# Kernel tuning notes

Hardware: AMD Instinct MI355X
Metric: run time of the kernel (lower is better)

Reference implementation:

```python
import jax, jax.numpy as jnp
import numpy as np

B, S, D, H = 2, 2048, 1024, 16
DH = D // H  # 64


def setup_inputs() -> dict:
    key = jax.random.key(0)
    ks = jax.random.split(key, 6)
    scale = 1.0 / np.sqrt(D)
    x = jax.random.normal(ks[0], (B, S, D), dtype=jnp.float32)
    Wq = jax.random.normal(ks[1], (D, D), dtype=jnp.float32) * scale
    Wk = jax.random.normal(ks[2], (D, D), dtype=jnp.float32) * scale
    Wv = jax.random.normal(ks[3], (D, D), dtype=jnp.float32) * scale
    Wo = jax.random.normal(ks[4], (D, D), dtype=jnp.float32) * scale
    zeros = jnp.zeros((D,), dtype=jnp.float32)
    return {"x": x, "Wq": Wq, "bq": zeros, "Wk": Wk, "bk": zeros,
            "Wv": Wv, "bv": zeros, "Wo": Wo, "bo": zeros}


def reference(x, Wq, bq, Wk, bk, Wv, bv, Wo, bo):
    # x: [B, S, D]
    def split_heads(t):
        # [B, S, D] -> [B, H, S, DH]
        return t.reshape(B, S, H, DH).transpose(0, 2, 1, 3)

    q = split_heads(x @ Wq + bq)
    k = split_heads(x @ Wk + bk)
    v = split_heads(x @ Wv + bv)

    scores = jnp.einsum('bhqd,bhkd->bhqk', q, k) / jnp.sqrt(jnp.float32(DH))
    weights = jax.nn.softmax(scores, axis=-1)          # [B, H, S, S]
    o = jnp.einsum('bhqk,bhkd->bhqd', weights, v)       # [B, H, S, DH]
    o = o.transpose(0, 2, 1, 3).reshape(B, S, D)        # merge heads
    return o @ Wo + bo
```

## Files before the change

### kernel.cpp

```cpp
#include <hip/hip_runtime.h>
#include <hip/hip_bf16.h>

#define DEV __device__ __forceinline__

typedef short bf16x8 __attribute__((ext_vector_type(8)));
typedef float f32x4 __attribute__((ext_vector_type(4)));
typedef unsigned int u32;
typedef unsigned int u32x4 __attribute__((ext_vector_type(4)));

constexpr int BB = 2, SS = 2048, DD = 1024, HH = 16, DHD = 64;
constexpr int MM = BB * SS;
#define QSC 0.1803368801111f

#if __has_builtin(__builtin_amdgcn_exp2f)
#define EXP2(x) __builtin_amdgcn_exp2f(x)
#else
#define EXP2(x) exp2f(x)
#endif

DEV unsigned short f2bf(float f) {
    union { float f; unsigned int u; } v; v.f = f;
    return (unsigned short)((v.u + 0x8000u) >> 16);
}
#if __has_builtin(__builtin_amdgcn_perm)
DEV u32 pk2bf(float a, float b) {
    union { float f; u32 u; } ua, ub; ua.f = a; ub.f = b;
    return __builtin_amdgcn_perm(ub.u + 0x8000u, ua.u + 0x8000u, 0x07060302u);
}
#else
DEV u32 pk2bf(float a, float b) {
    union { float f; u32 u; } ua, ub; ua.f = a; ub.f = b;
    return ((ua.u + 0x8000u) >> 16) | ((ub.u + 0x8000u) & 0xffff0000u);
}
#endif

DEV u32 cvtpk2bf(float a, float b) {
    u32 r;
    asm("v_cvt_pk_bf16_f32 %0, %1, %2" : "=v"(r) : "v"(a), "v"(b));
    return r;
}

DEV bf16x8 ld_bf16x8(const unsigned short* p) { return *(const bf16x8*)p; }

DEV void gl16(const unsigned short* g, unsigned short* l) {
    __builtin_amdgcn_global_load_lds(
        (const __attribute__((address_space(1))) u32*)g,
        (__attribute__((address_space(3))) u32*)l, 16, 0, 0);
}

__global__ void prep(const float* __restrict__ x, unsigned short* __restrict__ xb,
                     const float* __restrict__ W0, const float* __restrict__ W1,
                     const float* __restrict__ W2, const float* __restrict__ W3,
                     unsigned short* __restrict__ WtBase) {
    __shared__ float tile[32][33];
    int blk = blockIdx.x;
    if (blk < 4096) {
        int i = blk * 256 + threadIdx.x;
        float4 v = ((const float4*)x)[i];
        uint2 o;
        o.x = pk2bf(v.x, v.y);
        o.y = pk2bf(v.z, v.w);
        ((uint2*)xb)[i] = o;
        return;
    }
    blk -= 4096;
    int wsel = blk >> 10;
    const float* W = (wsel == 0) ? W0 : (wsel == 1) ? W1 : (wsel == 2) ? W2 : W3;
    unsigned short* Wt = WtBase + (size_t)wsel * DD * DD;
    int t = blk & 1023;
    int n0 = (t & 31) * 32, k0 = (t >> 5) * 32;
    int tx = threadIdx.x & 31, ty = threadIdx.x >> 5;
    #pragma unroll
    for (int i = 0; i < 4; ++i)
        tile[ty + 8 * i][tx] = W[(size_t)(k0 + ty + 8 * i) * DD + n0 + tx];
    __syncthreads();
    #pragma unroll
    for (int i = 0; i < 4; ++i)
        Wt[(size_t)(n0 + ty + 8 * i) * DD + k0 + tx] = f2bf(tile[tx][ty + 8 * i]);
}

__global__ __launch_bounds__(512, 2) void qkv_gemm(
    const unsigned short* __restrict__ xb,
    const unsigned short* __restrict__ WtBase,
    const float* __restrict__ bq, const float* __restrict__ bk, const float* __restrict__ bv,
    unsigned short* __restrict__ Qb, unsigned short* __restrict__ Kb, unsigned short* __restrict__ Vt)
{
    __shared__ __align__(16) unsigned short AL[3][128 * 32];
    __shared__ __align__(16) unsigned short BL[3][3][128 * 32];

    const int gid2 = blockIdx.x + 8 * blockIdx.y;
    const int xk = gid2 & 7, o = gid2 >> 3;
    const int xe = (xk & 1) * 4 + (o & 3);
    const int ye = (xk >> 1) * 8 + (o >> 2);
    const int m0g = ye * 128;
    const int n0g = xe * 128;

    const int wave = threadIdx.x >> 6, lane = threadIdx.x & 63;
    const int quad = lane >> 4, lcol = lane & 15;
    const int wr = wave >> 2, wc = wave & 3;

    f32x4 acc[3][4][2];
    #pragma unroll
    for (int z = 0; z < 3; ++z)
        #pragma unroll
        for (int i = 0; i < 4; ++i)
            #pragma unroll
            for (int j = 0; j < 2; ++j) acc[z][i][j] = (f32x4){0.f, 0.f, 0.f, 0.f};

    auto stage = [&](int ks, int bf) {
        int bi = threadIdx.x;
        int row = bi >> 2, p = (bi & 3) ^ ((row >> 1) & 3);
        gl16(xb + (size_t)(m0g + row) * DD + ks + p * 8, &AL[bf][wave * 512]);
        #pragma unroll
        for (int z = 0; z < 3; ++z)
            gl16(WtBase + (size_t)z * DD * DD + (size_t)(n0g + row) * DD + ks + p * 8,
                 &BL[bf][z][wave * 512]);
    };

    auto compute = [&](int bf) {
        bf16x8 af[4];
        #pragma unroll
        for (int mt = 0; mt < 4; ++mt) {
            int row = wr * 64 + mt * 16 + lcol;
            af[mt] = ld_bf16x8(&AL[bf][(row * 4 + (quad ^ ((row >> 1) & 3))) * 8]);
        }
        #pragma unroll
        for (int z = 0; z < 3; ++z) {
            bf16x8 bz[2];
            #pragma unroll
            for (int nt = 0; nt < 2; ++nt) {
                int row = wc * 32 + nt * 16 + lcol;
                bz[nt] = ld_bf16x8(&BL[bf][z][(row * 4 + (quad ^ ((row >> 1) & 3))) * 8]);
            }
            if (z < 2) {
                #pragma unroll
                for (int mt = 0; mt < 4; ++mt)
                    #pragma unroll
                    for (int nt = 0; nt < 2; ++nt)
                        acc[z][mt][nt] = __builtin_amdgcn_mfma_f32_16x16x32_bf16(bz[nt], af[mt], acc[z][mt][nt], 0, 0, 0);
            } else {
                #pragma unroll
                for (int mt = 0; mt < 4; ++mt)
                    #pragma unroll
                    for (int nt = 0; nt < 2; ++nt)
                        acc[z][mt][nt] = __builtin_amdgcn_mfma_f32_16x16x32_bf16(af[mt], bz[nt], acc[z][mt][nt], 0, 0, 0);
            }
        }
    };

    stage(0, 0);
    stage(32, 1);

    for (int kk = 0; kk < 30; kk += 3) {
        #pragma unroll
        for (int u = 0; u < 3; ++u) {
            int k = kk + u;
            stage((k + 2) * 32, (u + 2) % 3);
            asm volatile("s_waitcnt vmcnt(8)" ::: "memory");
            __builtin_amdgcn_s_barrier();
            __builtin_amdgcn_sched_barrier(0);
            compute(u);
            __builtin_amdgcn_s_barrier();
        }
    }
    asm volatile("s_waitcnt vmcnt(4)" ::: "memory");
    __builtin_amdgcn_s_barrier();
    __builtin_amdgcn_sched_barrier(0);
    compute(0);
    __builtin_amdgcn_s_barrier();
    asm volatile("s_waitcnt vmcnt(0)" ::: "memory");
    __builtin_amdgcn_s_barrier();
    __builtin_amdgcn_sched_barrier(0);
    compute(1);

    #pragma unroll
    for (int z = 0; z < 2; ++z) {
        unsigned short* dst = (z == 0) ? Qb : Kb;
        const float sc = (z == 0) ? QSC : 1.0f;
        const float* bias = (z == 0) ? bq : bk;
        #pragma unroll
        for (int mt = 0; mt < 4; ++mt) {
            int m = m0g + wr * 64 + mt * 16 + lcol;
            int b_ = m >> 11, s = m & (SS - 1);
            #pragma unroll
            for (int nt = 0; nt < 2; ++nt) {
                int nbt = n0g + wc * 32 + nt * 16 + quad * 4;
                int h = nbt >> 6, dh0 = nbt & 63;
                float4 bv4 = *(const float4*)&bias[nbt];
                uint2 o2;
                o2.x = pk2bf((acc[z][mt][nt][0] + bv4.x) * sc, (acc[z][mt][nt][1] + bv4.y) * sc);
                o2.y = pk2bf((acc[z][mt][nt][2] + bv4.z) * sc, (acc[z][mt][nt][3] + bv4.w) * sc);
                *(uint2*)&dst[(((size_t)b_ * HH + h) * SS + s) * DHD + dh0] = o2;
            }
        }
    }
    #pragma unroll
    for (int mt = 0; mt < 4; ++mt) {
        int mbt = m0g + wr * 64 + mt * 16 + quad * 4;
        int b_ = mbt >> 11, s0 = mbt & (SS - 1);
        #pragma unroll
        for (int nt = 0; nt < 2; ++nt) {
            int n = n0g + wc * 32 + nt * 16 + lcol;
            int h = n >> 6, dh = n & 63;
            float bvv = bv[n];
            uint2 o2;
            o2.x = pk2bf(acc[2][mt][nt][0] + bvv, acc[2][mt][nt][1] + bvv);
            o2.y = pk2bf(acc[2][mt][nt][2] + bvv, acc[2][mt][nt][3] + bvv);
            *(uint2*)&Vt[(((size_t)b_ * HH + h) * DHD + dh) * SS + s0] = o2;
        }
    }
}

__global__ __launch_bounds__(512, 4) void attn(
    const unsigned short* __restrict__ Qb,
    const unsigned short* __restrict__ Kb,
    const unsigned short* __restrict__ Vt,
    unsigned short* __restrict__ Ob)
{
    __shared__ __align__(16) unsigned short Kld[2][64 * 64];
    __shared__ __align__(16) unsigned short Vld[2][64 * 64];

    const int g = blockIdx.y * gridDim.x + blockIdx.x;
    const int bh = (g & 7) * 4 + ((g >> 3) & 3);
    const int qt = g >> 5;
    const int b = bh >> 4, h = bh & (HH - 1);
    const unsigned short* Qbh = Qb + (size_t)bh * SS * DHD;
    const unsigned short* Kbh = Kb + (size_t)bh * SS * DHD;
    const unsigned short* Vbh = Vt + (size_t)bh * DHD * SS;

    const int wave = threadIdx.x >> 6, lane = threadIdx.x & 63;
    const int quad = lane >> 4, lcol = lane & 15;
    const int rowbase = qt * 128 + wave * 16;

    bf16x8 qf0 = ld_bf16x8(Qbh + (size_t)(rowbase + lcol) * DHD + quad * 8);
    bf16x8 qf1 = ld_bf16x8(Qbh + (size_t)(rowbase + lcol) * DHD + 32 + quad * 8);

    auto krow = [&](int kf2, int j) {
        return kf2 * 32 + ((lcol >> 2) << 3) + j * 4 + (lcol & 3);
    };
    auto kswz = [](int r) { return (r & 3) | (((r >> 3) & 1) << 2); };

    auto stage = [&](int c, int bf) {
        int kb = c * 64;
        #pragma unroll
        for (int i = 0; i < 2; ++i) {
            int j = wave * 2 + i;
            if (j < 8) {
                int bi = j * 64 + lane;
                int r = bi >> 3, p = (bi & 7) ^ ((r & 3) | (((r >> 3) & 1) << 2));
                gl16(Kbh + (size_t)(kb + r) * DHD + p * 8, &Kld[bf][j * 512]);
            } else {
                int jj = j - 8;
                int bi = jj * 64 + lane;
                int dh = bi >> 3, p = (bi & 7) ^ (dh & 7);
                gl16(Vbh + (size_t)dh * SS + kb + p * 8, &Vld[bf][jj * 512]);
            }
        }
    };

    stage(0, 0);
    __syncthreads();

    float m0 = -1e30f;
    #pragma unroll
    for (int kf2 = 0; kf2 < 2; ++kf2)
        #pragma unroll
        for (int j = 0; j < 2; ++j) {
            int kr = krow(kf2, j), sw = kswz(kr);
            bf16x8 ka0 = ld_bf16x8(&Kld[0][(kr * 8 + (quad ^ sw)) * 8]);
            bf16x8 ka1 = ld_bf16x8(&Kld[0][(kr * 8 + ((quad + 4) ^ sw)) * 8]);
            f32x4 s = (f32x4){0.f, 0.f, 0.f, 0.f};
            s = __builtin_amdgcn_mfma_f32_16x16x32_bf16(ka0, qf0, s, 0, 0, 0);
            s = __builtin_amdgcn_mfma_f32_16x16x32_bf16(ka1, qf1, s, 0, 0, 0);
            #pragma unroll
            for (int r = 0; r < 4; ++r) m0 = fmaxf(m0, s[r]);
        }
    #pragma unroll
    for (int msk = 1; msk < 64; msk <<= 1) m0 = fmaxf(m0, __shfl_xor(m0, msk, 64));
    const f32x4 minit = (f32x4){-m0, -m0, -m0, -m0};

    f32x4 oacc[4];
    #pragma unroll
    for (int nt = 0; nt < 4; ++nt) oacc[nt] = (f32x4){0.f, 0.f, 0.f, 0.f};
    float ps = 0.f;

    for (int c = 0; c < 32; ++c) {
        int bf = c & 1;
        if (c + 1 < 32) stage(c + 1, (c + 1) & 1);

        bf16x8 paf[2];
        #pragma unroll
        for (int kf2 = 0; kf2 < 2; ++kf2) {
            u32 w[4];
            #pragma unroll
            for (int j = 0; j < 2; ++j) {
                int kr = krow(kf2, j), sw = kswz(kr);
                bf16x8 ka0 = ld_bf16x8(&Kld[bf][(kr * 8 + (quad ^ sw)) * 8]);
                bf16x8 ka1 = ld_bf16x8(&Kld[bf][(kr * 8 + ((quad + 4) ^ sw)) * 8]);
                f32x4 s = minit;
                s = __builtin_amdgcn_mfma_f32_16x16x32_bf16(ka0, qf0, s, 0, 0, 0);
                s = __builtin_amdgcn_mfma_f32_16x16x32_bf16(ka1, qf1, s, 0, 0, 0);
                float e0 = EXP2(s[0]), e1 = EXP2(s[1]);
                float e2 = EXP2(s[2]), e3 = EXP2(s[3]);
                ps += (e0 + e1) + (e2 + e3);
                w[j * 2]     = cvtpk2bf(e0, e1);
                w[j * 2 + 1] = cvtpk2bf(e2, e3);
            }
            union { u32x4 u; bf16x8 v; } pu;
            pu.u = (u32x4){w[0], w[1], w[2], w[3]};
            paf[kf2] = pu.v;
        }

        #pragma unroll
        for (int kf2 = 0; kf2 < 2; ++kf2) {
            #pragma unroll
            for (int nt = 0; nt < 4; ++nt) {
                int dh = nt * 16 + lcol;
                bf16x8 vb = ld_bf16x8(&Vld[bf][(dh * 8 + ((kf2 * 4 + quad) ^ (dh & 7))) * 8]);
                oacc[nt] = __builtin_amdgcn_mfma_f32_16x16x32_bf16(paf[kf2], vb, oacc[nt], 0, 0, 0);
            }
        }
        __syncthreads();
    }

    ps += __shfl_xor(ps, 16, 64);
    ps += __shfl_xor(ps, 32, 64);
    float inv = 1.0f / ps;
    #pragma unroll
    for (int r = 0; r < 4; ++r) {
        float iv = __shfl(inv, quad * 4 + r, 64);
        int srow = rowbase + quad * 4 + r;
        size_t base = (((size_t)b * SS + srow) * HH + h) * DHD;
        #pragma unroll
        for (int nt = 0; nt < 4; ++nt)
            Ob[base + nt * 16 + lcol] = f2bf(oacc[nt][r] * iv);
    }
}

__global__ __launch_bounds__(256) void out_gemm(
    const unsigned short* __restrict__ Ob,
    const unsigned short* __restrict__ Wto,
    const float* __restrict__ bo,
    float* __restrict__ out)
{
    __shared__ __align__(16) unsigned short Wld[2][128 * 64];
    __shared__ __align__(16) unsigned short Old[2][64 * 64];

    const int m0g = blockIdx.y * 64;
    const int n0g = blockIdx.x * 128;
    const int wave = threadIdx.x >> 6, lane = threadIdx.x & 63;
    const int quad = lane >> 4, lcol = lane & 15;
    const int nb = wave * 32;

    f32x4 acc[2][4];
    #pragma unroll
    for (int i = 0; i < 2; ++i)
        #pragma unroll
        for (int j = 0; j < 4; ++j) acc[i][j] = (f32x4){0.f, 0.f, 0.f, 0.f};

    auto stage = [&](int ks, int bf) {
        #pragma unroll
        for (int i = 0; i < 6; ++i) {
            int j = wave * 6 + i;
            if (j < 16) {
                int bi = j * 64 + lane;
                int r = bi >> 3, p = (bi & 7) ^ (r & 7);
                gl16(Wto + (size_t)(n0g + r) * DD + ks + p * 8, &Wld[bf][j * 512]);
            } else {
                int jj = j - 16;
                int bi = jj * 64 + lane;
                int r = bi >> 3, p = (bi & 7) ^ (r & 7);
                gl16(Ob + (size_t)(m0g + r) * DD + ks + p * 8, &Old[bf][jj * 512]);
            }
        }
    };

    stage(0, 0);
    __syncthreads();

    for (int kk = 0; kk < 16; ++kk) {
        int bf = kk & 1;
        if (kk + 1 < 16) stage((kk + 1) * 64, (kk + 1) & 1);
        #pragma unroll
        for (int kh = 0; kh < 2; ++kh) {
            bf16x8 wf[2], of[4];
            #pragma unroll
            for (int i = 0; i < 2; ++i) {
                int row = nb + i * 16 + lcol;
                wf[i] = ld_bf16x8(&Wld[bf][(row * 8 + ((kh * 4 + quad) ^ (row & 7))) * 8]);
            }
            #pragma unroll
            for (int j = 0; j < 4; ++j) {
                int row = j * 16 + lcol;
                of[j] = ld_bf16x8(&Old[bf][(row * 8 + ((kh * 4 + quad) ^ (row & 7))) * 8]);
            }
            #pragma unroll
            for (int i = 0; i < 2; ++i)
                #pragma unroll
                for (int j = 0; j < 4; ++j)
                    acc[i][j] = __builtin_amdgcn_mfma_f32_16x16x32_bf16(wf[i], of[j], acc[i][j], 0, 0, 0);
        }
        __syncthreads();
    }

    #pragma unroll
    for (int i = 0; i < 2; ++i) {
        int n4 = n0g + nb + i * 16 + quad * 4;
        float4 bv4 = *(const float4*)&bo[n4];
        #pragma unroll
        for (int j = 0; j < 4; ++j) {
            int token = m0g + j * 16 + lcol;
            float4 o;
            o.x = acc[i][j][0] + bv4.x;
            o.y = acc[i][j][1] + bv4.y;
            o.z = acc[i][j][2] + bv4.z;
            o.w = acc[i][j][3] + bv4.w;
            *(float4*)&out[(size_t)token * DD + n4] = o;
        }
    }
}

extern "C" void kernel_launch(void* const* d_in, const int* in_sizes, int n_in,
                              void* d_out, int out_size, void* d_ws, size_t ws_size,
                              hipStream_t stream)
{
    const float* x  = (const float*)d_in[0];
    const float* Wq = (const float*)d_in[1];
    const float* bq = (const float*)d_in[2];
    const float* Wk = (const float*)d_in[3];
    const float* bk = (const float*)d_in[4];
    const float* Wv = (const float*)d_in[5];
    const float* bv = (const float*)d_in[6];
    const float* Wo = (const float*)d_in[7];
    const float* bo = (const float*)d_in[8];
    float* out = (float*)d_out;

    unsigned short* ws = (unsigned short*)d_ws;
    unsigned short* Wt  = ws;
    unsigned short* Wto = Wt + 3 * (size_t)DD * DD;
    unsigned short* Qb  = Wt + 4 * (size_t)DD * DD;
    unsigned short* Kb  = Qb + (size_t)MM * DD;
    unsigned short* Vt  = Kb + (size_t)MM * DD;
    unsigned short* xb  = Vt + (size_t)MM * DD;
    unsigned short* Ob  = xb;

    prep<<<8192, 256, 0, stream>>>(x, xb, Wq, Wk, Wv, Wo, Wt);

    qkv_gemm<<<dim3(8, 32), 512, 0, stream>>>(xb, Wt, bq, bk, bv, Qb, Kb, Vt);

    attn<<<dim3(16, 32), 512, 0, stream>>>(Qb, Kb, Vt, Ob);

    out_gemm<<<dim3(DD / 128, MM / 64), 256, 0, stream>>>(Ob, Wto, bo, out);
}
```

Before: 183.7 us.

## Split attention key chunk across wave pairs, each wave handling 32 query rows

After: 198.1 us. 7.8% more time.

```diff
diff --git a/kernel.cpp b/kernel.cpp
--- a/kernel.cpp
+++ b/kernel.cpp
@@ -219,6 +219,9 @@
 {
     __shared__ __align__(16) unsigned short Kld[2][64 * 64];
     __shared__ __align__(16) unsigned short Vld[2][64 * 64];
+    __shared__ float exch[8 * 16 * 64];
+    __shared__ float psx[8][2][16];
+    __shared__ float smax[8];
 
     const int g = blockIdx.y * gridDim.x + blockIdx.x;
     const int bh = (g & 7) * 4 + ((g >> 3) & 3);
@@ -230,13 +233,18 @@
 
     const int wave = threadIdx.x >> 6, lane = threadIdx.x & 63;
     const int quad = lane >> 4, lcol = lane & 15;
-    const int rowbase = qt * 128 + wave * 16;
-
-    bf16x8 qf0 = ld_bf16x8(Qbh + (size_t)(rowbase + lcol) * DHD + quad * 8);
-    bf16x8 qf1 = ld_bf16x8(Qbh + (size_t)(rowbase + lcol) * DHD + 32 + quad * 8);
-
-    auto krow = [&](int kf2, int j) {
-        return kf2 * 32 + ((lcol >> 2) << 3) + j * 4 + (lcol & 3);
+    const int qg = wave >> 1, kh = wave & 1;
+    const int rowbase = qt * 128 + qg * 32;
+
+    bf16x8 qf0[2], qf1[2];
+    #pragma unroll
+    for (int g2 = 0; g2 < 2; ++g2) {
+        qf0[g2] = ld_bf16x8(Qbh + (size_t)(rowbase + g2 * 16 + lcol) * DHD + quad * 8);
+        qf1[g2] = ld_bf16x8(Qbh + (size_t)(rowbase + g2 * 16 + lcol) * DHD + 32 + quad * 8);
+    }
+
+    auto krow = [&](int j) {
+        return kh * 32 + ((lcol >> 2) << 3) + j * 4 + (lcol & 3);
     };
     auto kswz = [](int r) { return (r & 3) | (((r >> 3) & 1) << 2); };
 
@@ -260,80 +268,109 @@
 
     stage(0, 0);
     __syncthreads();
-
-    float m0 = -1e30f;
-    #pragma unroll
-    for (int kf2 = 0; kf2 < 2; ++kf2)
+    {
+        float m0 = -1e30f;
         #pragma unroll
         for (int j = 0; j < 2; ++j) {
-            int kr = krow(kf2, j), sw = kswz(kr);
+            int kr = krow(j), sw = kswz(kr);
             bf16x8 ka0 = ld_bf16x8(&Kld[0][(kr * 8 + (quad ^ sw)) * 8]);
             bf16x8 ka1 = ld_bf16x8(&Kld[0][(kr * 8 + ((quad + 4) ^ sw)) * 8]);
-            f32x4 s = (f32x4){0.f, 0.f, 0.f, 0.f};
-            s = __builtin_amdgcn_mfma_f32_16x16x32_bf16(ka0, qf0, s, 0, 0, 0);
-            s = __builtin_amdgcn_mfma_f32_16x16x32_bf16(ka1, qf1, s, 0, 0, 0);
-            #pragma unroll
-            for (int r = 0; r < 4; ++r) m0 = fmaxf(m0, s[r]);
-        }
-    #pragma unroll
-    for (int msk = 1; msk < 64; msk <<= 1) m0 = fmaxf(m0, __shfl_xor(m0, msk, 64));
-    const f32x4 minit = (f32x4){-m0, -m0, -m0, -m0};
-
-    f32x4 oacc[4];
-    #pragma unroll
-    for (int nt = 0; nt < 4; ++nt) oacc[nt] = (f32x4){0.f, 0.f, 0.f, 0.f};
-    float ps = 0.f;
+            #pragma unroll
+            for (int g2 = 0; g2 < 2; ++g2) {
+                f32x4 s = (f32x4){0.f, 0.f, 0.f, 0.f};
+                s = __builtin_amdgcn_mfma_f32_16x16x32_bf16(ka0, qf0[g2], s, 0, 0, 0);
+                s = __builtin_amdgcn_mfma_f32_16x16x32_bf16(ka1, qf1[g2], s, 0, 0, 0);
+                #pragma unroll
+                for (int r = 0; r < 4; ++r) m0 = fmaxf(m0, s[r]);
+            }
+        }
+        #pragma unroll
+        for (int msk = 1; msk < 64; msk <<= 1) m0 = fmaxf(m0, __shfl_xor(m0, msk, 64));
+        if (lane == 0) smax[wave] = m0;
+    }
+    __syncthreads();
+    float m0b = smax[0];
+    #pragma unroll
+    for (int w2 = 1; w2 < 8; ++w2) m0b = fmaxf(m0b, smax[w2]);
+    const f32x4 minit = (f32x4){-m0b, -m0b, -m0b, -m0b};
+
+    f32x4 oacc[2][4];
+    #pragma unroll
+    for (int g2 = 0; g2 < 2; ++g2)
+        #pragma unroll
+        for (int nt = 0; nt < 4; ++nt) oacc[g2][nt] = (f32x4){0.f, 0.f, 0.f, 0.f};
+    float ps0 = 0.f, ps1 = 0.f;
 
     for (int c = 0; c < 32; ++c) {
         int bf = c & 1;
         if (c + 1 < 32) stage(c + 1, (c + 1) & 1);
 
+        bf16x8 ka0[2], ka1[2];
+        #pragma unroll
+        for (int j = 0; j < 2; ++j) {
+            int kr = krow(j), sw = kswz(kr);
+            ka0[j] = ld_bf16x8(&Kld[bf][(kr * 8 + (quad ^ sw)) * 8]);
+            ka1[j] = ld_bf16x8(&Kld[bf][(kr * 8 + ((quad + 4) ^ sw)) * 8]);
+        }
         bf16x8 paf[2];
         #pragma unroll
-        for (int kf2 = 0; kf2 < 2; ++kf2) {
+        for (int g2 = 0; g2 < 2; ++g2) {
             u32 w[4];
             #pragma unroll
             for (int j = 0; j < 2; ++j) {
-                int kr = krow(kf2, j), sw = kswz(kr);
-                bf16x8 ka0 = ld_bf16x8(&Kld[bf][(kr * 8 + (quad ^ sw)) * 8]);
-                bf16x8 ka1 = ld_bf16x8(&Kld[bf][(kr * 8 + ((quad + 4) ^ sw)) * 8]);
                 f32x4 s = minit;
-                s = __builtin_amdgcn_mfma_f32_16x16x32_bf16(ka0, qf0, s, 0, 0, 0);
-                s = __builtin_amdgcn_mfma_f32_16x16x32_bf16(ka1, qf1, s, 0, 0, 0);
+                s = __builtin_amdgcn_mfma_f32_16x16x32_bf16(ka0[j], qf0[g2], s, 0, 0, 0);
+                s = __builtin_amdgcn_mfma_f32_16x16x32_bf16(ka1[j], qf1[g2], s, 0, 0, 0);
                 float e0 = EXP2(s[0]), e1 = EXP2(s[1]);
                 float e2 = EXP2(s[2]), e3 = EXP2(s[3]);
-                ps += (e0 + e1) + (e2 + e3);
+                if (g2 == 0) ps0 += (e0 + e1) + (e2 + e3);
+                else         ps1 += (e0 + e1) + (e2 + e3);
                 w[j * 2]     = cvtpk2bf(e0, e1);
                 w[j * 2 + 1] = cvtpk2bf(e2, e3);
             }
             union { u32x4 u; bf16x8 v; } pu;
             pu.u = (u32x4){w[0], w[1], w[2], w[3]};
-            paf[kf2] = pu.v;
-        }
-
-        #pragma unroll
-        for (int kf2 = 0; kf2 < 2; ++kf2) {
-            #pragma unroll
-            for (int nt = 0; nt < 4; ++nt) {
-                int dh = nt * 16 + lcol;
-                bf16x8 vb = ld_bf16x8(&Vld[bf][(dh * 8 + ((kf2 * 4 + quad) ^ (dh & 7))) * 8]);
-                oacc[nt] = __builtin_amdgcn_mfma_f32_16x16x32_bf16(paf[kf2], vb, oacc[nt], 0, 0, 0);
-            }
+            paf[g2] = pu.v;
+        }
+
+        #pragma unroll
+        for (int nt = 0; nt < 4; ++nt) {
+            int dh = nt * 16 + lcol;
+            bf16x8 vb = ld_bf16x8(&Vld[bf][(dh * 8 + ((kh * 4 + quad) ^ (dh & 7))) * 8]);
+            oacc[0][nt] = __builtin_amdgcn_mfma_f32_16x16x32_bf16(paf[0], vb, oacc[0][nt], 0, 0, 0);
+            oacc[1][nt] = __builtin_amdgcn_mfma_f32_16x16x32_bf16(paf[1], vb, oacc[1][nt], 0, 0, 0);
         }
         __syncthreads();
     }
 
-    ps += __shfl_xor(ps, 16, 64);
-    ps += __shfl_xor(ps, 32, 64);
-    float inv = 1.0f / ps;
-    #pragma unroll
-    for (int r = 0; r < 4; ++r) {
-        float iv = __shfl(inv, quad * 4 + r, 64);
-        int srow = rowbase + quad * 4 + r;
-        size_t base = (((size_t)b * SS + srow) * HH + h) * DHD;
-        #pragma unroll
-        for (int nt = 0; nt < 4; ++nt)
-            Ob[base + nt * 16 + lcol] = f2bf(oacc[nt][r] * iv);
+    ps0 += __shfl_xor(ps0, 16, 64); ps0 += __shfl_xor(ps0, 32, 64);
+    ps1 += __shfl_xor(ps1, 16, 64); ps1 += __shfl_xor(ps1, 32, 64);
+    if (lane < 16) { psx[wave][0][lane] = ps0; psx[wave][1][lane] = ps1; }
+    #pragma unroll
+    for (int g2 = 0; g2 < 2; ++g2)
+        #pragma unroll
+        for (int t = 0; t < 2; ++t)
+            #pragma unroll
+            for (int r = 0; r < 4; ++r)
+                exch[((wave * 16) + g2 * 8 + t * 4 + r) * 64 + lane] = oacc[g2][(kh ^ 1) * 2 + t][r];
+    __syncthreads();
+    const int pw = wave ^ 1;
+    #pragma unroll
+    for (int g2 = 0; g2 < 2; ++g2) {
+        #pragma unroll
+        for (int r = 0; r < 4; ++r) {
+            int q = quad * 4 + r;
+            float pstot = psx[qg * 2][g2][q] + psx[qg * 2 + 1][g2][q];
+            float iv = 1.0f / pstot;
+            int srow = rowbase + g2 * 16 + q;
+            size_t base = (((size_t)b * SS + srow) * HH + h) * DHD;
+            #pragma unroll
+            for (int t = 0; t < 2; ++t) {
+                int nt = kh * 2 + t;
+                float v = oacc[g2][nt][r] + exch[((pw * 16) + g2 * 8 + t * 4 + r) * 64 + lane];
+                Ob[base + nt * 16 + lcol] = f2bf(v * iv);
+            }
+        }
     }
 }
 
```

## Triple-buffer out_gemm with BK=32, vmcnt-based waits, and XCD-aware block remap

Applied to the files above, without the earlier changes.

Measured after the change: 183.4 us. About the same (-0.2%).

```diff
diff --git a/kernel.cpp b/kernel.cpp
--- a/kernel.cpp
+++ b/kernel.cpp
@@ -337,17 +337,22 @@
     }
 }
 
-__global__ __launch_bounds__(256) void out_gemm(
+__global__ __launch_bounds__(256, 4) void out_gemm(
     const unsigned short* __restrict__ Ob,
     const unsigned short* __restrict__ Wto,
     const float* __restrict__ bo,
     float* __restrict__ out)
 {
-    __shared__ __align__(16) unsigned short Wld[2][128 * 64];
-    __shared__ __align__(16) unsigned short Old[2][64 * 64];
-
-    const int m0g = blockIdx.y * 64;
-    const int n0g = blockIdx.x * 128;
+    __shared__ __align__(16) unsigned short Wld[3][128 * 32];
+    __shared__ __align__(16) unsigned short Old[3][64 * 32];
+
+    const int gid2 = blockIdx.x + 8 * blockIdx.y;
+    const int xk = gid2 & 7, o = gid2 >> 3;
+    const int xe = (xk & 1) * 4 + (o & 3);
+    const int ye = (xk >> 1) * 16 + (o >> 2);
+    const int m0g = ye * 64;
+    const int n0g = xe * 128;
+
     const int wave = threadIdx.x >> 6, lane = threadIdx.x & 63;
     const int quad = lane >> 4, lcol = lane & 15;
     const int nb = wave * 32;
@@ -360,48 +365,61 @@
 
     auto stage = [&](int ks, int bf) {
         #pragma unroll
-        for (int i = 0; i < 6; ++i) {
-            int j = wave * 6 + i;
-            if (j < 16) {
-                int bi = j * 64 + lane;
-                int r = bi >> 3, p = (bi & 7) ^ (r & 7);
-                gl16(Wto + (size_t)(n0g + r) * DD + ks + p * 8, &Wld[bf][j * 512]);
-            } else {
-                int jj = j - 16;
-                int bi = jj * 64 + lane;
-                int r = bi >> 3, p = (bi & 7) ^ (r & 7);
-                gl16(Ob + (size_t)(m0g + r) * DD + ks + p * 8, &Old[bf][jj * 512]);
-            }
-        }
+        for (int i = 0; i < 2; ++i) {
+            int bi = i * 256 + threadIdx.x;
+            int r = bi >> 2, p = (bi & 3) ^ ((r >> 1) & 3);
+            gl16(Wto + (size_t)(n0g + r) * DD + ks + p * 8, &Wld[bf][(i * 4 + wave) * 512]);
+        }
+        {
+            int bi = threadIdx.x;
+            int r = bi >> 2, p = (bi & 3) ^ ((r >> 1) & 3);
+            gl16(Ob + (size_t)(m0g + r) * DD + ks + p * 8, &Old[bf][wave * 512]);
+        }
+    };
+
+    auto compute = [&](int bf) {
+        bf16x8 wf[2], of[4];
+        #pragma unroll
+        for (int i = 0; i < 2; ++i) {
+            int row = nb + i * 16 + lcol;
+            wf[i] = ld_bf16x8(&Wld[bf][(row * 4 + (quad ^ ((row >> 1) & 3))) * 8]);
+        }
+        #pragma unroll
+        for (int j = 0; j < 4; ++j) {
+            int row = j * 16 + lcol;
+            of[j] = ld_bf16x8(&Old[bf][(row * 4 + (quad ^ ((row >> 1) & 3))) * 8]);
+        }
+        #pragma unroll
+        for (int i = 0; i < 2; ++i)
+            #pragma unroll
+            for (int j = 0; j < 4; ++j)
+                acc[i][j] = __builtin_amdgcn_mfma_f32_16x16x32_bf16(wf[i], of[j], acc[i][j], 0, 0, 0);
     };
 
     stage(0, 0);
-    __syncthreads();
-
-    for (int kk = 0; kk < 16; ++kk) {
-        int bf = kk & 1;
-        if (kk + 1 < 16) stage((kk + 1) * 64, (kk + 1) & 1);
-        #pragma unroll
-        for (int kh = 0; kh < 2; ++kh) {
-            bf16x8 wf[2], of[4];
-            #pragma unroll
-            for (int i = 0; i < 2; ++i) {
-                int row = nb + i * 16 + lcol;
-                wf[i] = ld_bf16x8(&Wld[bf][(row * 8 + ((kh * 4 + quad) ^ (row & 7))) * 8]);
-            }
-            #pragma unroll
-            for (int j = 0; j < 4; ++j) {
-                int row = j * 16 + lcol;
-                of[j] = ld_bf16x8(&Old[bf][(row * 8 + ((kh * 4 + quad) ^ (row & 7))) * 8]);
-            }
-            #pragma unroll
-            for (int i = 0; i < 2; ++i)
-                #pragma unroll
-                for (int j = 0; j < 4; ++j)
-                    acc[i][j] = __builtin_amdgcn_mfma_f32_16x16x32_bf16(wf[i], of[j], acc[i][j], 0, 0, 0);
-        }
-        __syncthreads();
-    }
+    stage(32, 1);
+
+    for (int kk = 0; kk < 30; kk += 3) {
+        #pragma unroll
+        for (int u = 0; u < 3; ++u) {
+            int k = kk + u;
+            stage((k + 2) * 32, (u + 2) % 3);
+            asm volatile("s_waitcnt vmcnt(6)" ::: "memory");
+            __builtin_amdgcn_s_barrier();
+            __builtin_amdgcn_sched_barrier(0);
+            compute(u);
+            __builtin_amdgcn_s_barrier();
+        }
+    }
+    asm volatile("s_waitcnt vmcnt(3)" ::: "memory");
+    __builtin_amdgcn_s_barrier();
+    __builtin_amdgcn_sched_barrier(0);
+    compute(0);
+    __builtin_amdgcn_s_barrier();
+    asm volatile("s_waitcnt vmcnt(0)" ::: "memory");
+    __builtin_amdgcn_s_barrier();
+    __builtin_amdgcn_sched_barrier(0);
+    compute(1);
 
     #pragma unroll
     for (int i = 0; i < 2; ++i) {
@@ -410,12 +428,12 @@
         #pragma unroll
         for (int j = 0; j < 4; ++j) {
             int token = m0g + j * 16 + lcol;
-            float4 o;
-            o.x = acc[i][j][0] + bv4.x;
-            o.y = acc[i][j][1] + bv4.y;
-            o.z = acc[i][j][2] + bv4.z;
-            o.w = acc[i][j][3] + bv4.w;
-            *(float4*)&out[(size_t)token * DD + n4] = o;
+            float4 o2;
+            o2.x = acc[i][j][0] + bv4.x;
+            o2.y = acc[i][j][1] + bv4.y;
+            o2.z = acc[i][j][2] + bv4.z;
+            o2.w = acc[i][j][3] + bv4.w;
+            *(float4*)&out[(size_t)token * DD + n4] = o2;
         }
     }
 }
@@ -450,5 +468,5 @@
 
     attn<<<dim3(16, 32), 512, 0, stream>>>(Qb, Kb, Vt, Ob);
 
-    out_gemm<<<dim3(DD / 128, MM / 64), 256, 0, stream>>>(Ob, Wto, bo, out);
-}
+    out_gemm<<<dim3(8, 64), 256, 0, stream>>>(Ob, Wto, bo, out);
+}
```
